# Kernel tuning notes

Hardware: AMD Instinct MI355X
Metric: run time of the kernel (lower is better)

Reference implementation:

```python
import jax, jax.numpy as jnp
import numpy as np

T, N, E = 4, 20000, 640000
D_IN, D_OUT = 256, 128
RRELU_SLOPE = (1.0 / 8.0 + 1.0 / 3.0) / 2.0  # RReLU eval-mode slope


def setup_inputs() -> dict:
    key = jax.random.key(0)
    ks = jax.random.split(key, 16)

    def glorot(k, shape):
        lim = np.sqrt(6.0 / (shape[0] + shape[1]))
        return jax.random.uniform(k, shape, jnp.float32, -lim, lim)

    node_embs = jax.random.normal(ks[0], (T, N, D_IN), jnp.float32)
    edge_index = jax.random.randint(ks[1], (T, 2, E), 0, N, jnp.int32)
    edge_weight = jax.random.uniform(ks[2], (T, E), jnp.float32)
    mask = jnp.zeros((T, N), jnp.float32)
    return {
        "node_embs": node_embs,
        "edge_index": edge_index,
        "edge_weight": edge_weight,
        "mask": mask,
        "p": glorot(ks[3], (D_IN, 1)),
        "Wz": glorot(ks[4], (D_IN, D_IN)),
        "Uz": glorot(ks[5], (D_IN, D_IN)),
        "bz": jnp.zeros((D_IN, D_OUT), jnp.float32),
        "Wr": glorot(ks[6], (D_IN, D_IN)),
        "Ur": glorot(ks[7], (D_IN, D_IN)),
        "br": jnp.zeros((D_IN, D_OUT), jnp.float32),
        "Wh": glorot(ks[8], (D_IN, D_IN)),
        "Uh": glorot(ks[9], (D_IN, D_IN)),
        "bh": jnp.zeros((D_IN, D_OUT), jnp.float32),
        "W0": glorot(ks[10], (D_IN, D_OUT)),
    }


def reference(node_embs, edge_index, edge_weight, mask, p, Wz, Uz, bz, Wr, Ur, br, Wh, Uh, bh, W0):
    n = node_embs.shape[1]
    k = W0.shape[1]

    def step(W, inputs):
        x, ei, w, m = inputs  # x: [N, D_IN]
        # --- TopK summary (EvolveGCN-H) ---
        scores = (x @ p)[:, 0] / jnp.linalg.norm(p) + m  # [N]
        vals, idx = jax.lax.top_k(scores, k)
        xt = (x[idx] * jnp.tanh(vals)[:, None]).T  # [D_IN, k]
        # --- matrix GRU cell: hidden state is the GCN weight W ---
        z = jax.nn.sigmoid(Wz @ xt + Uz @ W + bz)
        r = jax.nn.sigmoid(Wr @ xt + Ur @ W + br)
        h = jnp.tanh(Wh @ xt + Uh @ (r * W) + bh)
        Wn = (1.0 - z) * W + z * h  # [D_IN, D_OUT]
        # --- sparse GCN conv: adj @ (x @ Wn) ---
        y = x @ Wn  # [N, D_OUT]
        dst, src = ei[0], ei[1]
        agg = jax.ops.segment_sum(w[:, None] * y[src], dst, num_segments=n)
        out = jnp.where(agg >= 0, agg, RRELU_SLOPE * agg)
        return Wn, out

    _, out_seq = jax.lax.scan(step, W0, (node_embs, edge_index, edge_weight, mask))
    return out_seq  # [T, N, D_OUT]
```

## Files before the change

### kernel.cpp

```cpp
#include <hip/hip_runtime.h>

typedef unsigned short u16;
typedef unsigned int u32;
typedef unsigned long long u64;

#define T_ 4
#define N_ 20000
#define E_ 640000
#define DIN 256
#define DOUT 128
#define NT (T_*N_)
#define TE (T_*E_)
#define SLOPE 0.22916666666666666f

#define NB 125
#define BNODES 160
#define CAP 5632
#define NBTOT (T_*NB)

typedef __attribute__((ext_vector_type(8))) short short8;
typedef __attribute__((ext_vector_type(4))) float f32x4;

__device__ __forceinline__ float blo(u32 u) { return __uint_as_float(u << 16); }
__device__ __forceinline__ float bhi(u32 u) { return __uint_as_float(u & 0xFFFF0000u); }
__device__ __forceinline__ u16 f2bf(float f) {
    u32 u = __float_as_uint(f);
    return (u16)((u + 0x7FFFu + ((u >> 16) & 1u)) >> 16);
}
__device__ __forceinline__ u32 fkey(float f) {
    u32 u = __float_as_uint(f);
    return (u & 0x80000000u) ? ~u : (u | 0x80000000u);
}
__device__ __forceinline__ float fkeyinv(u32 k) {
    u32 u = (k & 0x80000000u) ? (k ^ 0x80000000u) : ~k;
    return __uint_as_float(u);
}

__global__ void k_transpose(const float* Wz, const float* Uz, const float* Wr, const float* Ur,
                            const float* Wh, const float* Uh, u32* Tp) {
    int bid = blockIdx.x;
    int m = bid >> 7, b = bid & 127;
    int idx = b * 256 + threadIdx.x;
    int d2 = idx & 127, i = idx >> 7;
    const float* src;
    switch (m) {
        case 0: src = Wz; break;
        case 1: src = Uz; break;
        case 2: src = Wr; break;
        case 3: src = Ur; break;
        case 4: src = Wh; break;
        default: src = Uh; break;
    }
    float lo = src[i * 256 + 2 * d2];
    float hi = src[i * 256 + 2 * d2 + 1];
    Tp[m * 32768 + d2 * 256 + i] = (u32)f2bf(lo) | ((u32)f2bf(hi) << 16);
}

__global__ __launch_bounds__(256) void k_scores(const float* x, const float* p, const float* mask,
                                                float* scores, u16* xb16) {
    __shared__ float pl[256];
    __shared__ float s_invn;
    int tid = threadIdx.x;
    pl[tid] = p[tid];
    __syncthreads();
    if (tid < 64) {
        float v = pl[tid] * pl[tid] + pl[tid + 64] * pl[tid + 64] +
                  pl[tid + 128] * pl[tid + 128] + pl[tid + 192] * pl[tid + 192];
        for (int o = 32; o > 0; o >>= 1) v += __shfl_xor(v, o);
        if (tid == 0) s_invn = 1.0f / sqrtf(v);
    }
    __syncthreads();
    int wid = tid >> 6, lane = tid & 63;
    for (int it = 0; it < 4; ++it) {
        int node = blockIdx.x * 16 + wid * 4 + it;
        const float* row = x + (size_t)node * DIN + lane * 4;
        float4 u = *(const float4*)row;
        float d = u.x * pl[lane * 4 + 0] + u.y * pl[lane * 4 + 1] +
                  u.z * pl[lane * 4 + 2] + u.w * pl[lane * 4 + 3];
        u32 p0 = (u32)f2bf(u.x) | ((u32)f2bf(u.y) << 16);
        u32 p1 = (u32)f2bf(u.z) | ((u32)f2bf(u.w) << 16);
        *(uint2*)(xb16 + (size_t)node * DIN + lane * 4) = make_uint2(p0, p1);
        for (int o = 32; o > 0; o >>= 1) d += __shfl_xor(d, o);
        if (lane == 0) scores[node] = d * s_invn + mask[node];
    }
}

__global__ __launch_bounds__(256) void k_bin(const int* ei, const float* ew,
                                             int* gcur, uint2* binned) {
    int blk = blockIdx.x;
    int t = blk / 250, ci = blk - t * 250;
    int ebase = ci * 2560;
    int tid = threadIdx.x;
    __shared__ u32 hist[128], sc[128], gbase[128];
    __shared__ uint2 stage[2560];
    if (tid < 128) hist[tid] = 0;
    __syncthreads();
    u32 px[10]; u32 pw[10]; u16 rk[10];
#pragma unroll
    for (int k = 0; k < 10; ++k) {
        int e = ebase + tid + k * 256;
        int dst = ei[t * (2 * E_) + e];
        int src = ei[t * (2 * E_) + E_ + e];
        float w = ew[t * E_ + e];
        int b = dst / BNODES;
        int dl = dst - b * BNODES;
        px[k] = (u32)(t * N_ + src) | ((u32)dl << 17) | ((u32)b << 25);
        pw[k] = __float_as_uint(w);
        rk[k] = (u16)atomicAdd(&hist[b], 1u);
    }
    __syncthreads();
    if (tid < 128) sc[tid] = hist[tid];
    __syncthreads();
    for (int o = 1; o < 128; o <<= 1) {
        u32 v = 0;
        if (tid < 128) { v = sc[tid]; if (tid >= o) v += sc[tid - o]; }
        __syncthreads();
        if (tid < 128) sc[tid] = v;
        __syncthreads();
    }
    if (tid < NB) gbase[tid] = (u32)atomicAdd(&gcur[t * NB + tid], (int)hist[tid]);
#pragma unroll
    for (int k = 0; k < 10; ++k) {
        int b = px[k] >> 25;
        u32 slot = (sc[b] - hist[b]) + rk[k];
        stage[slot] = make_uint2(px[k], pw[k]);
    }
    __syncthreads();
    for (int s = tid; s < 2560; s += 256) {
        uint2 v = stage[s];
        int b = v.x >> 25;
        u32 local = gbase[b] + ((u32)s - (sc[b] - hist[b]));
        if (local < CAP)
            binned[(size_t)(t * NB + b) * CAP + local] = v;
    }
}

__global__ __launch_bounds__(512) void k_scatter(const int* gcur, uint2* binned, int* offsets) {
    int bg = blockIdx.x;
    int t = bg / NB, bl = bg - t * NB;
    uint2* bucket = binned + (size_t)bg * CAP;
    int cnt = gcur[bg]; if (cnt > CAP) cnt = CAP;
    int tid = threadIdx.x;
    __shared__ u32 nhist[256], sc2[256], nstart[BNODES];
    if (tid < 256) nhist[tid] = 0;
    __syncthreads();
    u32 vx[11]; u32 vw[11]; u16 r_[11];
#pragma unroll
    for (int k = 0; k < 11; ++k) {
        int e = tid + k * 512;
        r_[k] = 0xFFFFu;
        if (e < cnt) {
            uint2 v = bucket[e];
            vx[k] = v.x; vw[k] = v.y;
            int dl = (v.x >> 17) & 255;
            r_[k] = (u16)atomicAdd(&nhist[dl], 1u);
        }
    }
    __syncthreads();
    if (tid < 256) sc2[tid] = nhist[tid];
    __syncthreads();
    for (int o = 1; o < 256; o <<= 1) {
        u32 v = 0;
        if (tid < 256) { v = sc2[tid]; if (tid >= o) v += sc2[tid - o]; }
        __syncthreads();
        if (tid < 256) sc2[tid] = v;
        __syncthreads();
    }
    if (tid < BNODES) {
        u32 st = sc2[tid] - nhist[tid];
        nstart[tid] = st;
        offsets[t * N_ + bl * BNODES + tid] = bg * CAP + (int)st;
    }
    if (bg == NBTOT - 1 && tid == 0) offsets[NT] = NBTOT * CAP;
    __syncthreads();
#pragma unroll
    for (int k = 0; k < 11; ++k) {
        if (r_[k] != 0xFFFFu) {
            int dl = (vx[k] >> 17) & 255;
            u32 pos = nstart[dl] + r_[k];
            bucket[pos] = make_uint2(vx[k] & 0x1FFFFu, vw[k]);
        }
    }
    for (int s = cnt + tid; s < CAP; s += 512) bucket[s] = make_uint2(0u, 0u);
}

__global__ __launch_bounds__(1024) void k_topk(const float* scores, const float* x, float* xtT) {
    int t = blockIdx.x;
    int tid = threadIdx.x;
    const float* sc = scores + t * N_;
    __shared__ u32 hist[256];
    __shared__ u32 sh_dig, sh_need;
    __shared__ u64 sel[256];
    __shared__ u32 selCount;
    __shared__ u32 idxl[128];
    __shared__ float tvl[128];

    u32 kreg[20];
#pragma unroll
    for (int p = 0; p < 20; ++p) {
        int i = tid + p * 1024;
        kreg[p] = (i < N_) ? fkey(sc[i]) : 0u;
    }

    u32 pref = 0;
    u32 need = 128;
    for (int pass = 0; pass < 4; ++pass) {
        int shift = 24 - 8 * pass;
        if (tid < 256) hist[tid] = 0;
        __syncthreads();
#pragma unroll
        for (int p = 0; p < 20; ++p) {
            int i = tid + p * 1024;
            u32 k = kreg[p];
            bool ok = (i < N_) && ((pass == 0) || ((k >> (shift + 8)) == pref));
            if (ok) atomicAdd(&hist[(k >> shift) & 255u], 1u);
        }
        __syncthreads();
        if (tid < 64) {
            int l = tid;
            u32 s = hist[4 * l] + hist[4 * l + 1] + hist[4 * l + 2] + hist[4 * l + 3];
            u32 S = s;
            for (int o = 1; o < 64; o <<= 1) {
                u32 y = __shfl_down(S, o);
                if (l + o < 64) S += y;
            }
            u64 m = __ballot(S >= need);
            int L = 63 - __builtin_clzll(m);
            if (l == L) {
                u32 Snext = S - s;
                u32 r = 0;
                for (int dd = 3; dd >= 0; --dd) {
                    u32 hb = hist[4 * L + dd];
                    r += hb;
                    if (Snext + r >= need) {
                        sh_dig = (u32)(4 * L + dd);
                        sh_need = need - (Snext + r - hb);
                        break;
                    }
                }
            }
        }
        __syncthreads();
        pref = (pref << 8) | sh_dig;
        need = sh_need;
        __syncthreads();
    }
    if (tid == 0) selCount = 0;
    __syncthreads();
    u32 theta = pref;
#pragma unroll
    for (int p = 0; p < 20; ++p) {
        int i = tid + p * 1024;
        u32 k = kreg[p];
        if (i < N_ && k >= theta) {
            u32 pos = atomicAdd(&selCount, 1u);
            if (pos < 256) sel[pos] = (((u64)(k ^ 0xFFFFFFFFu)) << 32) | (u32)i;
        }
    }
    __syncthreads();
    u32 c = selCount;
    if (c > 256) c = 256;
    if (tid < 256 && (u32)tid >= c) sel[tid] = 0xFFFFFFFFFFFFFFFFull;
    __syncthreads();
    for (int k2 = 2; k2 <= 256; k2 <<= 1) {
        for (int jj = k2 >> 1; jj > 0; jj >>= 1) {
            if (tid < 256) {
                int i = tid, ixj = i ^ jj;
                if (ixj > i) {
                    u64 A = sel[i], B = sel[ixj];
                    bool asc = ((i & k2) == 0);
                    bool sw = asc ? (A > B) : (A < B);
                    if (sw) { sel[i] = B; sel[ixj] = A; }
                }
            }
            __syncthreads();
        }
    }
    if (tid < 128) {
        u64 v = sel[tid];
        u32 k = ((u32)(v >> 32)) ^ 0xFFFFFFFFu;
        idxl[tid] = (u32)(v & 0xFFFFFFFFu);
        tvl[tid] = tanhf(fkeyinv(k));
    }
    __syncthreads();
    float* xt_t = xtT + t * (DIN * DOUT);
    const float* xb = x + (size_t)t * N_ * DIN;
    for (int e2 = tid; e2 < DIN * DOUT; e2 += 1024) {
        int j = e2 >> 8, d = e2 & 255;
        xt_t[e2] = xb[(size_t)idxl[j] * DIN + d] * tvl[j];
    }
}

__global__ __launch_bounds__(256) void k_gru(const float* xtT, const float* WprevT,
                                             const float* W0, int firstT, const u32* Tp,
                                             const float* bz, const float* br, const float* bh,
                                             float* WnextT, u16* WnT_t) {
    int j0 = blockIdx.x;
    int j1 = j0 + 64;
    int i = threadIdx.x;
    __shared__ float sxt[2][256], sW[2][256], srw[2][256];
    sxt[0][i] = xtT[j0 * 256 + i];
    sxt[1][i] = xtT[j1 * 256 + i];
    float wv0 = firstT ? W0[i * 128 + j0] : WprevT[j0 * 256 + i];
    float wv1 = firstT ? W0[i * 128 + j1] : WprevT[j1 * 256 + i];
    sW[0][i] = wv0;
    sW[1][i] = wv1;
    __syncthreads();
    const u32* WzT = Tp;
    const u32* UzT = Tp + 32768;
    const u32* WrT = Tp + 65536;
    const u32* UrT = Tp + 98304;
    const u32* WhT = Tp + 131072;
    const u32* UhT = Tp + 163840;
    float az0 = bz[i * 128 + j0], az1 = bz[i * 128 + j1];
    float ar0 = br[i * 128 + j0], ar1 = br[i * 128 + j1];
#pragma unroll 4
    for (int d2 = 0; d2 < 128; ++d2) {
        float x00 = sxt[0][2 * d2], x01 = sxt[0][2 * d2 + 1];
        float x10 = sxt[1][2 * d2], x11 = sxt[1][2 * d2 + 1];
        float w00 = sW[0][2 * d2], w01 = sW[0][2 * d2 + 1];
        float w10 = sW[1][2 * d2], w11 = sW[1][2 * d2 + 1];
        u32 a = WzT[d2 * 256 + i], b = UzT[d2 * 256 + i];
        u32 cc = WrT[d2 * 256 + i], dd = UrT[d2 * 256 + i];
        az0 += blo(a) * x00 + bhi(a) * x01 + blo(b) * w00 + bhi(b) * w01;
        az1 += blo(a) * x10 + bhi(a) * x11 + blo(b) * w10 + bhi(b) * w11;
        ar0 += blo(cc) * x00 + bhi(cc) * x01 + blo(dd) * w00 + bhi(dd) * w01;
        ar1 += blo(cc) * x10 + bhi(cc) * x11 + blo(dd) * w10 + bhi(dd) * w11;
    }
    float z0 = 1.0f / (1.0f + expf(-az0));
    float z1 = 1.0f / (1.0f + expf(-az1));
    float r0 = 1.0f / (1.0f + expf(-ar0));
    float r1 = 1.0f / (1.0f + expf(-ar1));
    srw[0][i] = r0 * wv0;
    srw[1][i] = r1 * wv1;
    __syncthreads();
    float ah0 = bh[i * 128 + j0], ah1 = bh[i * 128 + j1];
#pragma unroll 4
    for (int d2 = 0; d2 < 128; ++d2) {
        float x00 = sxt[0][2 * d2], x01 = sxt[0][2 * d2 + 1];
        float x10 = sxt[1][2 * d2], x11 = sxt[1][2 * d2 + 1];
        float r00 = srw[0][2 * d2], r01 = srw[0][2 * d2 + 1];
        float r10 = srw[1][2 * d2], r11 = srw[1][2 * d2 + 1];
        u32 a = WhT[d2 * 256 + i], b = UhT[d2 * 256 + i];
        ah0 += blo(a) * x00 + bhi(a) * x01 + blo(b) * r00 + bhi(b) * r01;
        ah1 += blo(a) * x10 + bhi(a) * x11 + blo(b) * r10 + bhi(b) * r11;
    }
    float h0 = tanhf(ah0), h1 = tanhf(ah1);
    float wn0 = (1.0f - z0) * wv0 + z0 * h0;
    float wn1 = (1.0f - z1) * wv1 + z1 * h1;
    WnextT[j0 * 256 + i] = wn0;
    WnextT[j1 * 256 + i] = wn1;
    WnT_t[j0 * 256 + i] = f2bf(wn0);
    WnT_t[j1 * 256 + i] = f2bf(wn1);
}

__global__ __launch_bounds__(128) void k_gemm(const u16* xb16, const u16* WnT, u16* y) {
    int t = blockIdx.y;
    const u16* xb = xb16 + (size_t)t * N_ * DIN;
    const u16* Bt = WnT + t * (DIN * DOUT);
    u16* yb = y + (size_t)t * N_ * DOUT;
    int wid = threadIdx.x >> 6, lane = threadIdx.x & 63;
    int quad = lane >> 4, lm = lane & 15;
    int rowBase = blockIdx.x * 64 + wid * 32;
    f32x4 acc[2][8];
#pragma unroll
    for (int mi = 0; mi < 2; ++mi)
#pragma unroll
        for (int ni = 0; ni < 8; ++ni) acc[mi][ni] = (f32x4){0.f, 0.f, 0.f, 0.f};
    size_t aoff[2];
#pragma unroll
    for (int mi = 0; mi < 2; ++mi) {
        int r = rowBase + mi * 16 + lm;
        if (r > N_ - 1) r = N_ - 1;
        aoff[mi] = (size_t)r * DIN + quad * 8;
    }
    const u16* bbase = Bt + lm * 256 + quad * 8;
    for (int kk = 0; kk < 256; kk += 32) {
        short8 a0 = *(const short8*)(xb + aoff[0] + kk);
        short8 a1 = *(const short8*)(xb + aoff[1] + kk);
#pragma unroll
        for (int ni = 0; ni < 8; ++ni) {
            short8 b = *(const short8*)(bbase + ni * 4096 + kk);
            acc[0][ni] = __builtin_amdgcn_mfma_f32_16x16x32_bf16(a0, b, acc[0][ni], 0, 0, 0);
            acc[1][ni] = __builtin_amdgcn_mfma_f32_16x16x32_bf16(a1, b, acc[1][ni], 0, 0, 0);
        }
    }
#pragma unroll
    for (int mi = 0; mi < 2; ++mi)
#pragma unroll
        for (int ni = 0; ni < 8; ++ni)
#pragma unroll
            for (int r = 0; r < 4; ++r) {
                int row = rowBase + mi * 16 + quad * 4 + r;
                if (row < N_) yb[(size_t)row * DOUT + ni * 16 + lm] = f2bf(acc[mi][ni][r]);
            }
}

__global__ __launch_bounds__(256) void k_agg(const int* offsets, const uint2* srcw,
                                             const u16* y, float* out) {
    int nb = (blockIdx.x & 7) * 2500 + (blockIdx.x >> 3);
    int g = nb * 4 + (threadIdx.x >> 6);
    int lane = threadIdx.x & 63;
    int q = lane >> 4, lq = lane & 15;
    int o0 = offsets[g], o1 = offsets[g + 1];
    float acc[8];
#pragma unroll
    for (int i = 0; i < 8; ++i) acc[i] = 0.f;
    int e0 = o0;
    for (; e0 + 8 <= o1; e0 += 8) {
        int ea = e0 + q, eb = e0 + 4 + q;
        uint2 ma = srcw[ea];
        uint2 mb = srcw[eb];
        float wa = __uint_as_float(ma.y);
        float wb = __uint_as_float(mb.y);
        uint4 va = *(const uint4*)(y + (size_t)ma.x * DOUT + lq * 8);
        uint4 vb = *(const uint4*)(y + (size_t)mb.x * DOUT + lq * 8);
        acc[0] += wa * blo(va.x); acc[1] += wa * bhi(va.x);
        acc[2] += wa * blo(va.y); acc[3] += wa * bhi(va.y);
        acc[4] += wa * blo(va.z); acc[5] += wa * bhi(va.z);
        acc[6] += wa * blo(va.w); acc[7] += wa * bhi(va.w);
        acc[0] += wb * blo(vb.x); acc[1] += wb * bhi(vb.x);
        acc[2] += wb * blo(vb.y); acc[3] += wb * bhi(vb.y);
        acc[4] += wb * blo(vb.z); acc[5] += wb * bhi(vb.z);
        acc[6] += wb * blo(vb.w); acc[7] += wb * bhi(vb.w);
    }
    for (; e0 < o1; e0 += 4) {
        int e = e0 + q;
        if (e < o1) {
            uint2 m = srcw[e];
            float wv = __uint_as_float(m.y);
            uint4 v = *(const uint4*)(y + (size_t)m.x * DOUT + lq * 8);
            acc[0] += wv * blo(v.x); acc[1] += wv * bhi(v.x);
            acc[2] += wv * blo(v.y); acc[3] += wv * bhi(v.y);
            acc[4] += wv * blo(v.z); acc[5] += wv * bhi(v.z);
            acc[6] += wv * blo(v.w); acc[7] += wv * bhi(v.w);
        }
    }
#pragma unroll
    for (int i = 0; i < 8; ++i) {
        acc[i] += __shfl_xor(acc[i], 16);
        acc[i] += __shfl_xor(acc[i], 32);
        acc[i] = (acc[i] >= 0.f) ? acc[i] : SLOPE * acc[i];
    }
    if (q == 0) {
        float4 v0 = make_float4(acc[0], acc[1], acc[2], acc[3]);
        float4 v1 = make_float4(acc[4], acc[5], acc[6], acc[7]);
        float* ob = out + (size_t)g * DOUT + lq * 8;
        *(float4*)ob = v0;
        *(float4*)(ob + 4) = v1;
    }
}

extern "C" void kernel_launch(void* const* d_in, const int* in_sizes, int n_in,
                              void* d_out, int out_size, void* d_ws, size_t ws_size,
                              hipStream_t stream) {
    const float* x = (const float*)d_in[0];
    const int* ei = (const int*)d_in[1];
    const float* ew = (const float*)d_in[2];
    const float* mask = (const float*)d_in[3];
    const float* p = (const float*)d_in[4];
    const float* Wz = (const float*)d_in[5];
    const float* Uz = (const float*)d_in[6];
    const float* bz = (const float*)d_in[7];
    const float* Wr = (const float*)d_in[8];
    const float* Ur = (const float*)d_in[9];
    const float* br = (const float*)d_in[10];
    const float* Wh = (const float*)d_in[11];
    const float* Uh = (const float*)d_in[12];
    const float* bh = (const float*)d_in[13];
    const float* W0 = (const float*)d_in[14];
    float* out = (float*)d_out;

    char* w = (char*)d_ws;
    u16* xb16 = (u16*)w;        w += (size_t)NT * DIN * 2;
    float* scores = (float*)w;  w += 320256;
    float* xtT = (float*)w;     w += 4 * 32768 * 4;
    float* Wst = (float*)w;     w += 2 * 32768 * 4;
    u16* WnT = (u16*)w;         w += 4 * 32768 * 2;
    u32* Tp = (u32*)w;          w += 6 * 32768 * 4;
    u16* y = (u16*)w;           w += (size_t)NT * DOUT * 2;
    uint2* binned = (uint2*)w;  w += (size_t)NBTOT * CAP * 8;
    int* gcur = (int*)w;        w += 2048;
    int* offsets = (int*)w;     w += 320256;

    hipMemsetAsync(gcur, 0, 2048, stream);

    k_transpose<<<768, 256, 0, stream>>>(Wz, Uz, Wr, Ur, Wh, Uh, Tp);
    k_scores<<<5000, 256, 0, stream>>>(x, p, mask, scores, xb16);
    k_bin<<<1000, 256, 0, stream>>>(ei, ew, gcur, binned);
    k_scatter<<<NBTOT, 512, 0, stream>>>(gcur, binned, offsets);
    k_topk<<<4, 1024, 0, stream>>>(scores, x, xtT);

    for (int t = 0; t < 4; ++t) {
        const float* WprevT = (t == 0) ? Wst : (Wst + ((t + 1) & 1) * 32768);
        float* WnextT = Wst + (t & 1) * 32768;
        k_gru<<<64, 256, 0, stream>>>(xtT + t * 32768, WprevT, W0, (t == 0) ? 1 : 0, Tp,
                                      bz, br, bh, WnextT, WnT + t * 32768);
    }
    k_gemm<<<dim3(313, 4), 128, 0, stream>>>(xb16, WnT, y);
    k_agg<<<N_, 256, 0, stream>>>(offsets, binned, y, out);
}
```

Baseline: 472.3 us.

## Sort edges by source sub-bin within each destination and unroll aggregation gather

The scatter kernel now bins edges by destination node and a coarse source-index range, so that each node's edge list is ordered by source region. This is meant to improve cache locality of the y-row gathers in the aggregation. The scatter prefix sum is replaced by a wave-shuffle scan over 2048 bins, fewer barriers than the old Hillis-Steele loop. The aggregation loop is unrolled to 16 edges per iteration so more gather loads are in flight, at the cost of more registers.

```diff
diff --git a/kernel.cpp b/kernel.cpp
--- a/kernel.cpp
+++ b/kernel.cpp
@@ -17,6 +17,11 @@
 #define BNODES 160
 #define CAP 5632
 #define NBTOT (T_*NB)
+
+#define SGRAN 11
+#define NSB 10
+#define NBIN (BNODES*NSB)
+#define NBIN_PAD 2048
 
 typedef __attribute__((ext_vector_type(8))) short short8;
 typedef __attribute__((ext_vector_type(4))) float f32x4;
@@ -141,10 +146,13 @@
     uint2* bucket = binned + (size_t)bg * CAP;
     int cnt = gcur[bg]; if (cnt > CAP) cnt = CAP;
     int tid = threadIdx.x;
-    __shared__ u32 nhist[256], sc2[256], nstart[BNODES];
-    if (tid < 256) nhist[tid] = 0;
-    __syncthreads();
-    u32 vx[11]; u32 vw[11]; u16 r_[11];
+    int tbase = t * N_;
+    __shared__ u32 nhist[NBIN_PAD];
+    __shared__ u32 binstart[NBIN_PAD];
+    __shared__ u32 wsum[8];
+    for (int i = tid; i < NBIN_PAD; i += 512) nhist[i] = 0;
+    __syncthreads();
+    u32 vx[11]; u32 vw[11]; u16 r_[11]; u16 bn_[11];
 #pragma unroll
     for (int k = 0; k < 11; ++k) {
         int e = tid + k * 512;
@@ -153,35 +161,46 @@
             uint2 v = bucket[e];
             vx[k] = v.x; vw[k] = v.y;
             int dl = (v.x >> 17) & 255;
-            r_[k] = (u16)atomicAdd(&nhist[dl], 1u);
-        }
-    }
-    __syncthreads();
-    if (tid < 256) sc2[tid] = nhist[tid];
-    __syncthreads();
-    for (int o = 1; o < 256; o <<= 1) {
-        u32 v = 0;
-        if (tid < 256) { v = sc2[tid]; if (tid >= o) v += sc2[tid - o]; }
-        __syncthreads();
-        if (tid < 256) sc2[tid] = v;
-        __syncthreads();
-    }
-    if (tid < BNODES) {
-        u32 st = sc2[tid] - nhist[tid];
-        nstart[tid] = st;
-        offsets[t * N_ + bl * BNODES + tid] = bg * CAP + (int)st;
-    }
+            int s = (int)(v.x & 0x1FFFFu) - tbase;
+            int bin = dl * NSB + (s >> SGRAN);
+            bn_[k] = (u16)bin;
+            r_[k] = (u16)atomicAdd(&nhist[bin], 1u);
+        }
+    }
+    __syncthreads();
+    u32 loc1, loc2, loc3, tsum;
+    {
+        int b0 = tid * 4;
+        u32 a = nhist[b0], b = nhist[b0 + 1], c = nhist[b0 + 2], d = nhist[b0 + 3];
+        loc1 = a; loc2 = a + b; loc3 = a + b + c; tsum = a + b + c + d;
+    }
+    int lane = tid & 63, wv = tid >> 6;
+    u32 xsc = tsum;
+    for (int o = 1; o < 64; o <<= 1) { u32 yv = __shfl_up(xsc, o); if (lane >= o) xsc += yv; }
+    if (lane == 63) wsum[wv] = xsc;
+    __syncthreads();
+    u32 wpre = 0;
+    for (int wq = 0; wq < wv; ++wq) wpre += wsum[wq];
+    u32 tpre = wpre + xsc - tsum;
+    {
+        int b0 = tid * 4;
+        binstart[b0] = tpre;
+        binstart[b0 + 1] = tpre + loc1;
+        binstart[b0 + 2] = tpre + loc2;
+        binstart[b0 + 3] = tpre + loc3;
+    }
+    __syncthreads();
+    if (tid < BNODES)
+        offsets[t * N_ + bl * BNODES + tid] = bg * CAP + (int)binstart[tid * NSB];
     if (bg == NBTOT - 1 && tid == 0) offsets[NT] = NBTOT * CAP;
-    __syncthreads();
 #pragma unroll
     for (int k = 0; k < 11; ++k) {
         if (r_[k] != 0xFFFFu) {
-            int dl = (vx[k] >> 17) & 255;
-            u32 pos = nstart[dl] + r_[k];
+            u32 pos = binstart[bn_[k]] + r_[k];
             bucket[pos] = make_uint2(vx[k] & 0x1FFFFu, vw[k]);
         }
     }
-    for (int s = cnt + tid; s < CAP; s += 512) bucket[s] = make_uint2(0u, 0u);
+    for (int s2 = cnt + tid; s2 < CAP; s2 += 512) bucket[s2] = make_uint2(0u, 0u);
 }
 
 __global__ __launch_bounds__(1024) void k_topk(const float* scores, const float* x, float* xtT) {
@@ -396,6 +415,12 @@
             }
 }
 
+#define ACC8(wv, v)                                             \
+    acc[0] += wv * blo(v.x); acc[1] += wv * bhi(v.x);           \
+    acc[2] += wv * blo(v.y); acc[3] += wv * bhi(v.y);           \
+    acc[4] += wv * blo(v.z); acc[5] += wv * bhi(v.z);           \
+    acc[6] += wv * blo(v.w); acc[7] += wv * bhi(v.w);
+
 __global__ __launch_bounds__(256) void k_agg(const int* offsets, const uint2* srcw,
                                              const u16* y, float* out) {
     int nb = (blockIdx.x & 7) * 2500 + (blockIdx.x >> 3);
@@ -407,22 +432,33 @@
 #pragma unroll
     for (int i = 0; i < 8; ++i) acc[i] = 0.f;
     int e0 = o0;
+    for (; e0 + 16 <= o1; e0 += 16) {
+        uint2 m0 = srcw[e0 + q];
+        uint2 m1 = srcw[e0 + 4 + q];
+        uint2 m2 = srcw[e0 + 8 + q];
+        uint2 m3 = srcw[e0 + 12 + q];
+        uint4 v0 = *(const uint4*)(y + (size_t)m0.x * DOUT + lq * 8);
+        uint4 v1 = *(const uint4*)(y + (size_t)m1.x * DOUT + lq * 8);
+        uint4 v2 = *(const uint4*)(y + (size_t)m2.x * DOUT + lq * 8);
+        uint4 v3 = *(const uint4*)(y + (size_t)m3.x * DOUT + lq * 8);
+        float w0 = __uint_as_float(m0.y);
+        float w1 = __uint_as_float(m1.y);
+        float w2 = __uint_as_float(m2.y);
+        float w3 = __uint_as_float(m3.y);
+        ACC8(w0, v0)
+        ACC8(w1, v1)
+        ACC8(w2, v2)
+        ACC8(w3, v3)
+    }
     for (; e0 + 8 <= o1; e0 += 8) {
-        int ea = e0 + q, eb = e0 + 4 + q;
-        uint2 ma = srcw[ea];
-        uint2 mb = srcw[eb];
+        uint2 ma = srcw[e0 + q];
+        uint2 mb = srcw[e0 + 4 + q];
+        uint4 va = *(const uint4*)(y + (size_t)ma.x * DOUT + lq * 8);
+        uint4 vb = *(const uint4*)(y + (size_t)mb.x * DOUT + lq * 8);
         float wa = __uint_as_float(ma.y);
         float wb = __uint_as_float(mb.y);
-        uint4 va = *(const uint4*)(y + (size_t)ma.x * DOUT + lq * 8);
-        uint4 vb = *(const uint4*)(y + (size_t)mb.x * DOUT + lq * 8);
-        acc[0] += wa * blo(va.x); acc[1] += wa * bhi(va.x);
-        acc[2] += wa * blo(va.y); acc[3] += wa * bhi(va.y);
-        acc[4] += wa * blo(va.z); acc[5] += wa * bhi(va.z);
-        acc[6] += wa * blo(va.w); acc[7] += wa * bhi(va.w);
-        acc[0] += wb * blo(vb.x); acc[1] += wb * bhi(vb.x);
-        acc[2] += wb * blo(vb.y); acc[3] += wb * bhi(vb.y);
-        acc[4] += wb * blo(vb.z); acc[5] += wb * bhi(vb.z);
-        acc[6] += wb * blo(vb.w); acc[7] += wb * bhi(vb.w);
+        ACC8(wa, va)
+        ACC8(wb, vb)
     }
     for (; e0 < o1; e0 += 4) {
         int e = e0 + q;
@@ -430,10 +466,7 @@
             uint2 m = srcw[e];
             float wv = __uint_as_float(m.y);
             uint4 v = *(const uint4*)(y + (size_t)m.x * DOUT + lq * 8);
-            acc[0] += wv * blo(v.x); acc[1] += wv * bhi(v.x);
-            acc[2] += wv * blo(v.y); acc[3] += wv * bhi(v.y);
-            acc[4] += wv * blo(v.z); acc[5] += wv * bhi(v.z);
-            acc[6] += wv * blo(v.w); acc[7] += wv * bhi(v.w);
+            ACC8(wv, v)
         }
     }
 #pragma unroll
```

Result: faster. 462.1 us (-2.2%).
